# Kernel optimization log

Hardware: AMD Instinct MI355X
Metric: run time of the kernel (lower is better)

## Reference

```python
import jax, jax.numpy as jnp
import numpy as np

HEADS = 16
DIM_HEAD = 64
DIM = 1024
EPS = 1e-5


def _layernorm(x, g, b):
    mu = jnp.mean(x, axis=-1, keepdims=True)
    var = jnp.var(x, axis=-1, keepdims=True)
    return (x - mu) * jax.lax.rsqrt(var + EPS) * g + b


def setup_inputs() -> dict:
    key = jax.random.key(0)
    ks = jax.random.split(key, 8)
    inner = HEADS * DIM_HEAD  # 1024
    x = jax.random.normal(ks[0], (2, 2048, DIM), dtype=jnp.float32)
    w_qkv = jax.random.normal(ks[1], (DIM, inner * 3), dtype=jnp.float32) * (DIM ** -0.5)
    w_out = jax.random.normal(ks[2], (inner, DIM), dtype=jnp.float32) * (inner ** -0.5)
    ln1_g = jnp.ones((DIM,), jnp.float32)
    ln1_b = jnp.zeros((DIM,), jnp.float32)
    ln2_g = jnp.ones((DIM,), jnp.float32)
    ln2_b = jnp.zeros((DIM,), jnp.float32)
    return {"x": x, "ln1_g": ln1_g, "ln1_b": ln1_b, "w_qkv": w_qkv,
            "w_out": w_out, "ln2_g": ln2_g, "ln2_b": ln2_b}


def reference(x, ln1_g, ln1_b, w_qkv, w_out, ln2_g, ln2_b):
    b, n, _ = x.shape
    scale = DIM_HEAD ** -0.5
    xn = _layernorm(x, ln1_g, ln1_b)
    qkv = xn @ w_qkv  # [b, n, 3*inner]
    q, k, v = jnp.split(qkv, 3, axis=-1)
    # b n (h d) -> b h n d
    resh = lambda t: t.reshape(b, n, HEADS, DIM_HEAD).transpose(0, 2, 1, 3)
    q, k, v = resh(q) * scale, resh(k), resh(v)
    sim = jnp.einsum('bhid,bhjd->bhij', q, k)
    causal = jnp.tril(jnp.ones((n, n), dtype=bool))
    # masked_fill(triu(1), 0) followed by relu == relu masked to lower triangle
    attn = jnp.where(causal, jax.nn.relu(sim), 0.0)
    out = jnp.einsum('bhij,bhjd->bhid', attn, v)
    out = out.transpose(0, 2, 1, 3).reshape(b, n, HEADS * DIM_HEAD)
    return _layernorm(out @ w_out, ln2_g, ln2_b)
```

## Files before the change

kernel.cpp:

```cpp
#include <hip/hip_runtime.h>
#include <cstdint>
#include <cstddef>


typedef __bf16 bf16_t;
typedef __bf16 bf16x8 __attribute__((ext_vector_type(8)));
typedef __bf16 bf16x4 __attribute__((ext_vector_type(4)));
typedef float  f32x4  __attribute__((ext_vector_type(4)));

#define DEV_INLINE __device__ __forceinline__

DEV_INLINE void async_copy16(void* lds, const void* g) {
  __builtin_amdgcn_global_load_lds(
      (__attribute__((address_space(1))) void*)(g),
      (__attribute__((address_space(3))) void*)(lds), 16, 0, 0);
}

__global__ __launch_bounds__(256) void ln1_kernel(
    const float* __restrict__ x, const float* __restrict__ g,
    const float* __restrict__ bta, bf16_t* __restrict__ xn) {
  const int row = blockIdx.x;
  const int t = threadIdx.x, w = t >> 6, l = t & 63;
  const float* xr = x + (size_t)row * 1024;
  float4 v = *(const float4*)(xr + t * 4);
  float s  = v.x + v.y + v.z + v.w;
  float s2 = v.x * v.x + v.y * v.y + v.z * v.z + v.w * v.w;
  #pragma unroll
  for (int off = 32; off >= 1; off >>= 1) {
    s  += __shfl_down(s, off);
    s2 += __shfl_down(s2, off);
  }
  __shared__ float red[8];
  if (l == 0) { red[w] = s; red[4 + w] = s2; }
  __syncthreads();
  s  = red[0] + red[1] + red[2] + red[3];
  s2 = red[4] + red[5] + red[6] + red[7];
  float mu  = s * (1.0f / 1024.0f);
  float var = s2 * (1.0f / 1024.0f) - mu * mu;
  float rs  = rsqrtf(var + 1e-5f);
  float4 gv = *(const float4*)(g + t * 4);
  float4 bv = *(const float4*)(bta + t * 4);
  bf16x4 o;
  o[0] = (bf16_t)((v.x - mu) * rs * gv.x + bv.x);
  o[1] = (bf16_t)((v.y - mu) * rs * gv.y + bv.y);
  o[2] = (bf16_t)((v.z - mu) * rs * gv.z + bv.z);
  o[3] = (bf16_t)((v.w - mu) * rs * gv.w + bv.w);
  *(bf16x4*)(xn + (size_t)row * 1024 + t * 4) = o;
}

__global__ __launch_bounds__(256) void ln2_kernel(
    const float* __restrict__ z0, const float* __restrict__ z1,
    const float* __restrict__ g, const float* __restrict__ bta,
    float* __restrict__ out) {
  const int row = blockIdx.x;
  const int t = threadIdx.x, w = t >> 6, l = t & 63;
  float4 v  = *(const float4*)(z0 + (size_t)row * 1024 + t * 4);
  float4 v1 = *(const float4*)(z1 + (size_t)row * 1024 + t * 4);
  v.x += v1.x; v.y += v1.y; v.z += v1.z; v.w += v1.w;
  float s  = v.x + v.y + v.z + v.w;
  float s2 = v.x * v.x + v.y * v.y + v.z * v.z + v.w * v.w;
  #pragma unroll
  for (int off = 32; off >= 1; off >>= 1) {
    s  += __shfl_down(s, off);
    s2 += __shfl_down(s2, off);
  }
  __shared__ float red[8];
  if (l == 0) { red[w] = s; red[4 + w] = s2; }
  __syncthreads();
  s  = red[0] + red[1] + red[2] + red[3];
  s2 = red[4] + red[5] + red[6] + red[7];
  float mu  = s * (1.0f / 1024.0f);
  float var = s2 * (1.0f / 1024.0f) - mu * mu;
  float rs  = rsqrtf(var + 1e-5f);
  float4 gv = *(const float4*)(g + t * 4);
  float4 bv = *(const float4*)(bta + t * 4);
  float4 o;
  o.x = (v.x - mu) * rs * gv.x + bv.x;
  o.y = (v.y - mu) * rs * gv.y + bv.y;
  o.z = (v.z - mu) * rs * gv.z + bv.z;
  o.w = (v.w - mu) * rs * gv.w + bv.w;
  *(float4*)(out + (size_t)row * 1024 + t * 4) = o;
}

__global__ __launch_bounds__(256) void wtrans_kernel(
    const float* __restrict__ wsrc, bf16_t* __restrict__ wdstT, int N) {
  __shared__ __align__(16) float tl[64][68];
  const int n0 = blockIdx.x * 64, k0 = blockIdx.y * 64;
  const int t = threadIdx.x;
  #pragma unroll
  for (int c = 0; c < 4; ++c) {
    int idx = c * 256 + t;
    int r = idx >> 4, c4 = (idx & 15) * 4;
    *(float4*)&tl[r][c4] = *(const float4*)(wsrc + (size_t)(k0 + r) * N + n0 + c4);
  }
  __syncthreads();
  #pragma unroll
  for (int c = 0; c < 2; ++c) {
    int idx = c * 256 + t;
    int nl = idx >> 3, kc = (idx & 7) * 8;
    bf16x8 o;
    #pragma unroll
    for (int ii = 0; ii < 8; ++ii) o[ii] = (bf16_t)tl[kc + ii][nl];
    *(bf16x8*)(wdstT + (size_t)(n0 + nl) * 1024 + k0 + kc) = o;
  }
}

__global__ __launch_bounds__(256) void vtrans_kernel(
    const bf16_t* __restrict__ v, bf16_t* __restrict__ vT) {
  __shared__ __align__(16) bf16_t tl[64][72];
  const int n0 = blockIdx.x * 64;
  const size_t bh = blockIdx.y;
  const int t = threadIdx.x;
  #pragma unroll
  for (int c = 0; c < 2; ++c) {
    int idx = c * 256 + t;
    int r = idx >> 3, c8 = (idx & 7) * 8;
    *(bf16x8*)&tl[r][c8] = *(const bf16x8*)(v + (bh * 2048 + n0 + r) * 64 + c8);
  }
  __syncthreads();
  #pragma unroll
  for (int c = 0; c < 2; ++c) {
    int idx = c * 256 + t;
    int d = idx >> 3, nc = (idx & 7) * 8;
    bf16x8 o;
    #pragma unroll
    for (int ii = 0; ii < 8; ++ii) o[ii] = tl[nc + ii][d];
    *(bf16x8*)(vT + (bh * 64 + d) * 2048 + n0 + nc) = o;
  }
}

template <int EPI, int KSPLIT>
__global__ __launch_bounds__(256, 3) void gemm128_kernel(
    const bf16_t* __restrict__ A, const bf16_t* __restrict__ Bt,
    void* __restrict__ C0, void* __restrict__ C1, void* __restrict__ C2) {
  __shared__ __align__(16) bf16_t As[128 * 64];
  __shared__ __align__(16) bf16_t Bs[128 * 64];
  const int t = threadIdx.x;
  const int w = t >> 6, l = t & 63, l15 = l & 15, quad = l >> 4;
  const int wy = w >> 1, wx = w & 1;
  const int m0 = blockIdx.y * 128, n0 = blockIdx.x * 128;
  const int kz = (KSPLIT > 1) ? blockIdx.z : 0;
  const int kt0 = kz * (16 / KSPLIT), kt1 = kt0 + (16 / KSPLIT);

  const int r_l = l >> 3;
  const int u_src = (l & 7) ^ r_l;
  const int rswz = l15 & 7;

  f32x4 acc[4][4];
  #pragma unroll
  for (int i = 0; i < 4; ++i)
    #pragma unroll
    for (int j = 0; j < 4; ++j) acc[i][j] = (f32x4)0.0f;

  for (int kt = kt0; kt < kt1; ++kt) {
    __syncthreads();
    #pragma unroll
    for (int c = 0; c < 4; ++c) {
      int idx = w * 4 + c;
      int row = idx * 8 + r_l;
      async_copy16(&As[idx * 512], A + (size_t)(m0 + row) * 1024 + kt * 64 + u_src * 8);
      async_copy16(&Bs[idx * 512], Bt + (size_t)(n0 + row) * 1024 + kt * 64 + u_src * 8);
    }
    __syncthreads();
    #pragma unroll
    for (int kk = 0; kk < 2; ++kk) {
      bf16x8 af[4], bfr[4];
      #pragma unroll
      for (int i = 0; i < 4; ++i)
        af[i] = *(const bf16x8*)&As[(wy * 64 + i * 16 + l15) * 64 + (((kk * 4 + quad) ^ rswz) * 8)];
      #pragma unroll
      for (int j = 0; j < 4; ++j)
        bfr[j] = *(const bf16x8*)&Bs[(wx * 64 + j * 16 + l15) * 64 + (((kk * 4 + quad) ^ rswz) * 8)];
      #pragma unroll
      for (int i = 0; i < 4; ++i)
        #pragma unroll
        for (int j = 0; j < 4; ++j)
          acc[i][j] = __builtin_amdgcn_mfma_f32_16x16x32_bf16(af[i], bfr[j], acc[i][j], 0, 0, 0);
    }
  }

  if (EPI == 0) {
    float* C = (float*)(kz == 0 ? C0 : C1);
    #pragma unroll
    for (int i = 0; i < 4; ++i)
      #pragma unroll
      for (int j = 0; j < 4; ++j)
        #pragma unroll
        for (int r = 0; r < 4; ++r) {
          int m = m0 + wy * 64 + i * 16 + quad * 4 + r;
          int n = n0 + wx * 64 + j * 16 + l15;
          C[(size_t)m * 1024 + n] = acc[i][j][r];
        }
  } else {
    int nb = n0 + wx * 64;
    int which = nb >> 10;
    int head = (nb & 1023) >> 6;
    bf16_t* dst = which == 0 ? (bf16_t*)C0 : which == 1 ? (bf16_t*)C1 : (bf16_t*)C2;
    float sc = which == 0 ? 0.125f : 1.0f;
    #pragma unroll
    for (int i = 0; i < 4; ++i)
      #pragma unroll
      for (int j = 0; j < 4; ++j)
        #pragma unroll
        for (int r = 0; r < 4; ++r) {
          int m = m0 + wy * 64 + i * 16 + quad * 4 + r;
          int bq = m >> 11, pos = m & 2047;
          int d = j * 16 + l15;
          dst[(((size_t)(bq * 16 + head)) * 2048 + pos) * 64 + d] =
              (bf16_t)(acc[i][j][r] * sc);
        }
  }
}

__global__ __launch_bounds__(256, 2) void attn_kernel(
    const bf16_t* __restrict__ q, const bf16_t* __restrict__ k,
    const bf16_t* __restrict__ vT, bf16_t* __restrict__ out) {
  __shared__ __align__(16) bf16_t Ks[2][128 * 64];
  __shared__ __align__(16) bf16_t Vts[2][128 * 64];
  __shared__ __align__(16) bf16_t Ss[64 * 72];

  const int h = blockIdx.x, p = blockIdx.y, b = blockIdx.z;
  const int t = threadIdx.x;
  const int w = t >> 6, l = t & 63, l15 = l & 15, quad = l >> 4;
  const size_t bh = (size_t)(b * 16 + h);
  const int tB = 31 - p;

  const int r_l = l >> 3;
  const int u_g = (l & 7) ^ r_l;
  const int rswz = l15 & 7;

  auto stage_tile = [&](int buf, int half, int kt2) {
    #pragma unroll
    for (int c = 0; c < 2; ++c) {
      int idx = w * 2 + c;
      int row = idx * 8 + r_l;
      async_copy16(&Ks[buf][half * 4096 + idx * 512],
                   k + (bh * 2048 + kt2 * 64 + row) * 64 + u_g * 8);
      async_copy16(&Vts[buf][half * 4096 + idx * 512],
                   vT + (bh * 64 + row) * 2048 + kt2 * 64 + u_g * 8);
    }
  };
  auto stage_it = [&](int it, int buf) {
    if (it <= p) {
      stage_tile(buf, 0, it);
    } else {
      int base = p + 1 + 2 * (it - p - 1);
      stage_tile(buf, 0, base);
      int k2 = base + 1; if (k2 > 31) k2 = 31;
      stage_tile(buf, 1, k2);
    }
  };

  auto load_lds = [&](const bf16_t* Kb, const bf16_t* Vb,
                      bf16x8 (&bk)[2][4], bf16x8 (&bv)[2][4]) {
    #pragma unroll
    for (int kk = 0; kk < 2; ++kk)
      #pragma unroll
      for (int tj = 0; tj < 4; ++tj) {
        int u = ((kk * 4 + quad) ^ rswz) * 8;
        bk[kk][tj] = *(const bf16x8*)&Kb[(tj * 16 + l15) * 64 + u];
        bv[kk][tj] = *(const bf16x8*)&Vb[(tj * 16 + l15) * 64 + u];
      }
  };

  bf16x8 qa[2][2];
  {
    int rA = p * 64 + w * 16, rB = tB * 64 + w * 16;
    #pragma unroll
    for (int kk = 0; kk < 2; ++kk) {
      qa[0][kk] = *(const bf16x8*)(q + (bh * 2048 + rA + l15) * 64 + kk * 32 + quad * 8);
      qa[1][kk] = *(const bf16x8*)(q + (bh * 2048 + rB + l15) * 64 + kk * 32 + quad * 8);
    }
  }

  f32x4 acc0[4], acc1[4];
  #pragma unroll
  for (int tj = 0; tj < 4; ++tj) { acc0[tj] = (f32x4)0.0f; acc1[tj] = (f32x4)0.0f; }

  auto unit = [&](f32x4 (&accr)[4], bf16x8 (&qf)[2],
                  bf16x8 (&bk)[2][4], bf16x8 (&bv)[2][4], bool dg) {
    f32x4 sacc[4];
    #pragma unroll
    for (int tj = 0; tj < 4; ++tj) sacc[tj] = (f32x4)0.0f;
    #pragma unroll
    for (int kk = 0; kk < 2; ++kk)
      #pragma unroll
      for (int tj = 0; tj < 4; ++tj)
        sacc[tj] = __builtin_amdgcn_mfma_f32_16x16x32_bf16(qf[kk], bk[kk][tj], sacc[tj], 0, 0, 0);
    #pragma unroll
    for (int tj = 0; tj < 4; ++tj)
      #pragma unroll
      for (int r = 0; r < 4; ++r) {
        float v = fmaxf(sacc[tj][r], 0.0f);
        if (dg && (tj * 16 + l15 > w * 16 + quad * 4 + r)) v = 0.0f;
        Ss[(w * 16 + quad * 4 + r) * 72 + tj * 16 + l15] = (bf16_t)v;
      }
    #pragma unroll
    for (int kk = 0; kk < 2; ++kk) {
      bf16x8 as_ = *(const bf16x8*)&Ss[(w * 16 + l15) * 72 + kk * 32 + quad * 8];
      #pragma unroll
      for (int tj = 0; tj < 4; ++tj)
        accr[tj] = __builtin_amdgcn_mfma_f32_16x16x32_bf16(as_, bv[kk][tj], accr[tj], 0, 0, 0);
    }
  };

  stage_it(0, 0);
  for (int it = 0; it < 17; ++it) {
    __syncthreads();
    if (it + 1 < 17) stage_it(it + 1, (it + 1) & 1);
    const int buf = it & 1;
    bf16x8 bk[2][4], bv[2][4];
    load_lds(&Ks[buf][0], &Vts[buf][0], bk, bv);
    if (it <= p) {
      unit(acc0, qa[0], bk, bv, it == p);
      unit(acc1, qa[1], bk, bv, false);
    } else {
      int base = p + 1 + 2 * (it - p - 1);
      unit(acc1, qa[1], bk, bv, base == tB);
      if (base + 1 <= tB) {
        load_lds(&Ks[buf][4096], &Vts[buf][4096], bk, bv);
        unit(acc1, qa[1], bk, bv, base + 1 == tB);
      }
    }
  }

  #pragma unroll
  for (int tj = 0; tj < 4; ++tj)
    #pragma unroll
    for (int r = 0; r < 4; ++r) {
      int col = h * 64 + tj * 16 + l15;
      int posA = p * 64 + w * 16 + quad * 4 + r;
      int posB = tB * 64 + w * 16 + quad * 4 + r;
      out[((size_t)b * 2048 + posA) * 1024 + col] = (bf16_t)acc0[tj][r];
      out[((size_t)b * 2048 + posB) * 1024 + col] = (bf16_t)acc1[tj][r];
    }
}

extern "C" void kernel_launch(void* const* d_in, const int* in_sizes, int n_in,
                              void* d_out, int out_size, void* d_ws, size_t ws_size,
                              hipStream_t stream) {
  (void)in_sizes; (void)n_in; (void)out_size; (void)ws_size;
  const float* x     = (const float*)d_in[0];
  const float* ln1_g = (const float*)d_in[1];
  const float* ln1_b = (const float*)d_in[2];
  const float* w_qkv = (const float*)d_in[3];
  const float* w_out = (const float*)d_in[4];
  const float* ln2_g = (const float*)d_in[5];
  const float* ln2_b = (const float*)d_in[6];
  float* out = (float*)d_out;

  char* ws = (char*)d_ws;
  bf16_t* xn     = (bf16_t*)(ws + 0);
  bf16_t* wqkvT  = (bf16_t*)(ws + 8388608);
  bf16_t* woutT  = (bf16_t*)(ws + 14680064);
  bf16_t* qb     = (bf16_t*)(ws + 16777216);
  bf16_t* kb     = (bf16_t*)(ws + 25165824);
  bf16_t* vb     = (bf16_t*)(ws + 33554432);
  bf16_t* vTb    = (bf16_t*)(ws + 41943040);
  bf16_t* ao     = (bf16_t*)(ws + 50331648);
  float*  z0     = (float*)(ws + 58720256);
  float*  z1     = (float*)(ws + 16777216);

  ln1_kernel<<<4096, 256, 0, stream>>>(x, ln1_g, ln1_b, xn);
  wtrans_kernel<<<dim3(48, 16), 256, 0, stream>>>(w_qkv, wqkvT, 3072);
  wtrans_kernel<<<dim3(16, 16), 256, 0, stream>>>(w_out, woutT, 1024);
  gemm128_kernel<1, 1><<<dim3(24, 32), 256, 0, stream>>>(xn, wqkvT, qb, kb, vb);
  vtrans_kernel<<<dim3(32, 32), 256, 0, stream>>>(vb, vTb);
  attn_kernel<<<dim3(16, 16, 2), 256, 0, stream>>>(qb, kb, vTb, ao);
  gemm128_kernel<0, 2><<<dim3(8, 32, 2), 256, 0, stream>>>(ao, woutT, z0, z1, nullptr);
  ln2_kernel<<<4096, 256, 0, stream>>>(z0, z1, ln2_g, ln2_b, out);
}
```

Measured before the change: 186.8 us.

## Merge prep kernels, store split-K partials as bf16, transpose attention MFMA outputs

Folds the LN1 kernel and both weight-transpose kernels into one launch with a block-index dispatch, cutting launch overhead. The split-K partial sums from the output projection are now stored as bf16 instead of fp32, halving that intermediate traffic, at some cost in precision. In attention, the MFMA operands are swapped so each lane holds a row of consecutive outputs. This allows packed bf16x4 stores to LDS and global memory instead of scattered scalar stores.

```diff
diff --git a/kernel.cpp b/kernel.cpp
--- a/kernel.cpp
+++ b/kernel.cpp
@@ -16,47 +16,79 @@
       (__attribute__((address_space(3))) void*)(lds), 16, 0, 0);
 }
 
-__global__ __launch_bounds__(256) void ln1_kernel(
-    const float* __restrict__ x, const float* __restrict__ g,
-    const float* __restrict__ bta, bf16_t* __restrict__ xn) {
-  const int row = blockIdx.x;
-  const int t = threadIdx.x, w = t >> 6, l = t & 63;
-  const float* xr = x + (size_t)row * 1024;
-  float4 v = *(const float4*)(xr + t * 4);
-  float s  = v.x + v.y + v.z + v.w;
-  float s2 = v.x * v.x + v.y * v.y + v.z * v.z + v.w * v.w;
-  #pragma unroll
-  for (int off = 32; off >= 1; off >>= 1) {
-    s  += __shfl_down(s, off);
-    s2 += __shfl_down(s2, off);
-  }
-  __shared__ float red[8];
-  if (l == 0) { red[w] = s; red[4 + w] = s2; }
-  __syncthreads();
-  s  = red[0] + red[1] + red[2] + red[3];
-  s2 = red[4] + red[5] + red[6] + red[7];
-  float mu  = s * (1.0f / 1024.0f);
-  float var = s2 * (1.0f / 1024.0f) - mu * mu;
-  float rs  = rsqrtf(var + 1e-5f);
-  float4 gv = *(const float4*)(g + t * 4);
-  float4 bv = *(const float4*)(bta + t * 4);
-  bf16x4 o;
-  o[0] = (bf16_t)((v.x - mu) * rs * gv.x + bv.x);
-  o[1] = (bf16_t)((v.y - mu) * rs * gv.y + bv.y);
-  o[2] = (bf16_t)((v.z - mu) * rs * gv.z + bv.z);
-  o[3] = (bf16_t)((v.w - mu) * rs * gv.w + bv.w);
-  *(bf16x4*)(xn + (size_t)row * 1024 + t * 4) = o;
+__global__ __launch_bounds__(256) void prep_kernel(
+    const float* __restrict__ x, const float* __restrict__ g1,
+    const float* __restrict__ b1, bf16_t* __restrict__ xn,
+    const float* __restrict__ w_qkv, bf16_t* __restrict__ wqkvT,
+    const float* __restrict__ w_out, bf16_t* __restrict__ woutT) {
+  const int bid = blockIdx.x;
+  const int t = threadIdx.x;
+  if (bid < 4096) {
+    const int w = t >> 6, l = t & 63;
+    const float* xr = x + (size_t)bid * 1024;
+    float4 v = *(const float4*)(xr + t * 4);
+    float s  = v.x + v.y + v.z + v.w;
+    float s2 = v.x * v.x + v.y * v.y + v.z * v.z + v.w * v.w;
+    #pragma unroll
+    for (int off = 32; off >= 1; off >>= 1) {
+      s  += __shfl_down(s, off);
+      s2 += __shfl_down(s2, off);
+    }
+    __shared__ float red[8];
+    if (l == 0) { red[w] = s; red[4 + w] = s2; }
+    __syncthreads();
+    s  = red[0] + red[1] + red[2] + red[3];
+    s2 = red[4] + red[5] + red[6] + red[7];
+    float mu  = s * (1.0f / 1024.0f);
+    float var = s2 * (1.0f / 1024.0f) - mu * mu;
+    float rs  = rsqrtf(var + 1e-5f);
+    float4 gv = *(const float4*)(g1 + t * 4);
+    float4 bv = *(const float4*)(b1 + t * 4);
+    bf16x4 o;
+    o[0] = (bf16_t)((v.x - mu) * rs * gv.x + bv.x);
+    o[1] = (bf16_t)((v.y - mu) * rs * gv.y + bv.y);
+    o[2] = (bf16_t)((v.z - mu) * rs * gv.z + bv.z);
+    o[3] = (bf16_t)((v.w - mu) * rs * gv.w + bv.w);
+    *(bf16x4*)(xn + (size_t)bid * 1024 + t * 4) = o;
+  } else {
+    const float* wsrc; bf16_t* wdst; int N, tile;
+    if (bid < 4864) { wsrc = w_qkv; wdst = wqkvT; N = 3072; tile = bid - 4096; }
+    else            { wsrc = w_out; wdst = woutT; N = 1024; tile = bid - 4864; }
+    const int ntiles = N >> 6;
+    const int n0 = (tile % ntiles) * 64, k0 = (tile / ntiles) * 64;
+    __shared__ __align__(16) float tl[64][68];
+    #pragma unroll
+    for (int c = 0; c < 4; ++c) {
+      int idx = c * 256 + t;
+      int r = idx >> 4, c4 = (idx & 15) * 4;
+      *(float4*)&tl[r][c4] = *(const float4*)(wsrc + (size_t)(k0 + r) * N + n0 + c4);
+    }
+    __syncthreads();
+    #pragma unroll
+    for (int c = 0; c < 2; ++c) {
+      int idx = c * 256 + t;
+      int nl = idx >> 3, kc = (idx & 7) * 8;
+      bf16x8 o;
+      #pragma unroll
+      for (int ii = 0; ii < 8; ++ii) o[ii] = (bf16_t)tl[kc + ii][nl];
+      *(bf16x8*)(wdst + (size_t)(n0 + nl) * 1024 + k0 + kc) = o;
+    }
+  }
 }
 
 __global__ __launch_bounds__(256) void ln2_kernel(
-    const float* __restrict__ z0, const float* __restrict__ z1,
+    const bf16_t* __restrict__ z0, const bf16_t* __restrict__ z1,
     const float* __restrict__ g, const float* __restrict__ bta,
     float* __restrict__ out) {
   const int row = blockIdx.x;
   const int t = threadIdx.x, w = t >> 6, l = t & 63;
-  float4 v  = *(const float4*)(z0 + (size_t)row * 1024 + t * 4);
-  float4 v1 = *(const float4*)(z1 + (size_t)row * 1024 + t * 4);
-  v.x += v1.x; v.y += v1.y; v.z += v1.z; v.w += v1.w;
+  bf16x4 a0 = *(const bf16x4*)(z0 + (size_t)row * 1024 + t * 4);
+  bf16x4 a1 = *(const bf16x4*)(z1 + (size_t)row * 1024 + t * 4);
+  float4 v;
+  v.x = (float)a0[0] + (float)a1[0];
+  v.y = (float)a0[1] + (float)a1[1];
+  v.z = (float)a0[2] + (float)a1[2];
+  v.w = (float)a0[3] + (float)a1[3];
   float s  = v.x + v.y + v.z + v.w;
   float s2 = v.x * v.x + v.y * v.y + v.z * v.z + v.w * v.w;
   #pragma unroll
@@ -82,29 +114,6 @@
   *(float4*)(out + (size_t)row * 1024 + t * 4) = o;
 }
 
-__global__ __launch_bounds__(256) void wtrans_kernel(
-    const float* __restrict__ wsrc, bf16_t* __restrict__ wdstT, int N) {
-  __shared__ __align__(16) float tl[64][68];
-  const int n0 = blockIdx.x * 64, k0 = blockIdx.y * 64;
-  const int t = threadIdx.x;
-  #pragma unroll
-  for (int c = 0; c < 4; ++c) {
-    int idx = c * 256 + t;
-    int r = idx >> 4, c4 = (idx & 15) * 4;
-    *(float4*)&tl[r][c4] = *(const float4*)(wsrc + (size_t)(k0 + r) * N + n0 + c4);
-  }
-  __syncthreads();
-  #pragma unroll
-  for (int c = 0; c < 2; ++c) {
-    int idx = c * 256 + t;
-    int nl = idx >> 3, kc = (idx & 7) * 8;
-    bf16x8 o;
-    #pragma unroll
-    for (int ii = 0; ii < 8; ++ii) o[ii] = (bf16_t)tl[kc + ii][nl];
-    *(bf16x8*)(wdstT + (size_t)(n0 + nl) * 1024 + k0 + kc) = o;
-  }
-}
-
 __global__ __launch_bounds__(256) void vtrans_kernel(
     const bf16_t* __restrict__ v, bf16_t* __restrict__ vT) {
   __shared__ __align__(16) bf16_t tl[64][72];
@@ -180,7 +189,7 @@
   }
 
   if (EPI == 0) {
-    float* C = (float*)(kz == 0 ? C0 : C1);
+    bf16_t* C = (bf16_t*)(kz == 0 ? C0 : C1);
     #pragma unroll
     for (int i = 0; i < 4; ++i)
       #pragma unroll
@@ -189,7 +198,7 @@
         for (int r = 0; r < 4; ++r) {
           int m = m0 + wy * 64 + i * 16 + quad * 4 + r;
           int n = n0 + wx * 64 + j * 16 + l15;
-          C[(size_t)m * 1024 + n] = acc[i][j][r];
+          C[(size_t)m * 1024 + n] = (bf16_t)acc[i][j][r];
         }
   } else {
     int nb = n0 + wx * 64;
@@ -286,21 +295,24 @@
     for (int kk = 0; kk < 2; ++kk)
       #pragma unroll
       for (int tj = 0; tj < 4; ++tj)
-        sacc[tj] = __builtin_amdgcn_mfma_f32_16x16x32_bf16(qf[kk], bk[kk][tj], sacc[tj], 0, 0, 0);
-    #pragma unroll
-    for (int tj = 0; tj < 4; ++tj)
+        sacc[tj] = __builtin_amdgcn_mfma_f32_16x16x32_bf16(bk[kk][tj], qf[kk], sacc[tj], 0, 0, 0);
+    #pragma unroll
+    for (int tj = 0; tj < 4; ++tj) {
+      bf16x4 pk;
       #pragma unroll
       for (int r = 0; r < 4; ++r) {
         float v = fmaxf(sacc[tj][r], 0.0f);
-        if (dg && (tj * 16 + l15 > w * 16 + quad * 4 + r)) v = 0.0f;
-        Ss[(w * 16 + quad * 4 + r) * 72 + tj * 16 + l15] = (bf16_t)v;
+        if (dg && (tj * 16 + quad * 4 + r > w * 16 + l15)) v = 0.0f;
+        pk[r] = (bf16_t)v;
       }
+      *(bf16x4*)&Ss[(w * 16 + l15) * 72 + tj * 16 + quad * 4] = pk;
+    }
     #pragma unroll
     for (int kk = 0; kk < 2; ++kk) {
       bf16x8 as_ = *(const bf16x8*)&Ss[(w * 16 + l15) * 72 + kk * 32 + quad * 8];
       #pragma unroll
       for (int tj = 0; tj < 4; ++tj)
-        accr[tj] = __builtin_amdgcn_mfma_f32_16x16x32_bf16(as_, bv[kk][tj], accr[tj], 0, 0, 0);
+        accr[tj] = __builtin_amdgcn_mfma_f32_16x16x32_bf16(bv[kk][tj], as_, accr[tj], 0, 0, 0);
     }
   };
 
@@ -325,15 +337,16 @@
   }
 
   #pragma unroll
-  for (int tj = 0; tj < 4; ++tj)
-    #pragma unroll
-    for (int r = 0; r < 4; ++r) {
-      int col = h * 64 + tj * 16 + l15;
-      int posA = p * 64 + w * 16 + quad * 4 + r;
-      int posB = tB * 64 + w * 16 + quad * 4 + r;
-      out[((size_t)b * 2048 + posA) * 1024 + col] = (bf16_t)acc0[tj][r];
-      out[((size_t)b * 2048 + posB) * 1024 + col] = (bf16_t)acc1[tj][r];
-    }
+  for (int tj = 0; tj < 4; ++tj) {
+    bf16x4 p0, p1;
+    #pragma unroll
+    for (int r = 0; r < 4; ++r) { p0[r] = (bf16_t)acc0[tj][r]; p1[r] = (bf16_t)acc1[tj][r]; }
+    int posA = p * 64 + w * 16 + l15;
+    int posB = tB * 64 + w * 16 + l15;
+    int col = h * 64 + tj * 16 + quad * 4;
+    *(bf16x4*)(out + ((size_t)b * 2048 + posA) * 1024 + col) = p0;
+    *(bf16x4*)(out + ((size_t)b * 2048 + posB) * 1024 + col) = p1;
+  }
 }
 
 extern "C" void kernel_launch(void* const* d_in, const int* in_sizes, int n_in,
@@ -358,15 +371,13 @@
   bf16_t* vb     = (bf16_t*)(ws + 33554432);
   bf16_t* vTb    = (bf16_t*)(ws + 41943040);
   bf16_t* ao     = (bf16_t*)(ws + 50331648);
-  float*  z0     = (float*)(ws + 58720256);
-  float*  z1     = (float*)(ws + 16777216);
-
-  ln1_kernel<<<4096, 256, 0, stream>>>(x, ln1_g, ln1_b, xn);
-  wtrans_kernel<<<dim3(48, 16), 256, 0, stream>>>(w_qkv, wqkvT, 3072);
-  wtrans_kernel<<<dim3(16, 16), 256, 0, stream>>>(w_out, woutT, 1024);
+  bf16_t* zb0    = (bf16_t*)(ws + 58720256);
+  bf16_t* zb1    = (bf16_t*)(ws + 67108864);
+
+  prep_kernel<<<5120, 256, 0, stream>>>(x, ln1_g, ln1_b, xn, w_qkv, wqkvT, w_out, woutT);
   gemm128_kernel<1, 1><<<dim3(24, 32), 256, 0, stream>>>(xn, wqkvT, qb, kb, vb);
   vtrans_kernel<<<dim3(32, 32), 256, 0, stream>>>(vb, vTb);
   attn_kernel<<<dim3(16, 16, 2), 256, 0, stream>>>(qb, kb, vTb, ao);
-  gemm128_kernel<0, 2><<<dim3(8, 32, 2), 256, 0, stream>>>(ao, woutT, z0, z1, nullptr);
-  ln2_kernel<<<4096, 256, 0, stream>>>(z0, z1, ln2_g, ln2_b, out);
-}
+  gemm128_kernel<0, 2><<<dim3(8, 32, 2), 256, 0, stream>>>(ao, woutT, zb0, zb1, nullptr);
+  ln2_kernel<<<4096, 256, 0, stream>>>(zb0, zb1, ln2_g, ln2_b, out);
+}
```

After: 178.6 us. -4.4%, faster.
